# Kernel optimization log

Hardware: AMD Instinct MI355X
Metric: run time of the kernel (lower is better)

## Reference

```python
import jax, jax.numpy as jnp
import numpy as np

B, S, H = 32, 4096, 1024


def setup_inputs() -> dict:
    key = jax.random.key(0)
    ks = jax.random.split(key, 6)
    sc = 1.0 / np.sqrt(H)
    return {
        "hidden_state": jax.random.normal(ks[0], (B, 1, H), dtype=jnp.float32),
        "encoder_outputs": jax.random.normal(ks[1], (B, S, H), dtype=jnp.float32),
        "A_w": jax.random.normal(ks[2], (H, H), dtype=jnp.float32) * sc,
        "A_b": jax.random.normal(ks[3], (H,), dtype=jnp.float32) * 0.01,
        "C_w": jax.random.normal(ks[4], (H, 2 * H), dtype=jnp.float32) * sc,
        "C_b": jax.random.normal(ks[5], (H,), dtype=jnp.float32) * 0.01,
    }


def reference(hidden_state, encoder_outputs, A_w, A_b, C_w, C_b):
    # NOTE: source applies A twice to hidden_state (first reassignment, then
    # again inside the bmm). We reproduce that exactly.
    h1 = hidden_state @ A_w.T + A_b            # [B,1,H] (reassigned hidden_state)
    h2 = h1 @ A_w.T + A_b                      # second A application for scores
    scores = jnp.einsum('bsh,bqh->bsq', encoder_outputs, h2)   # [B,S,1]
    attn = jax.nn.softmax(scores, axis=1)                      # softmax over S
    context = jnp.einsum('bsq,bsh->bqh', attn, encoder_outputs)  # [B,1,H]
    concat = jnp.concatenate([h1[:, 0], context[:, 0]], axis=1)  # [B,2H]
    out = jnp.tanh(concat @ C_w.T + C_b)                         # [B,H]
    return out, attn
```

## Files before the change

### kernel.cpp

```cpp
#include <hip/hip_runtime.h>
#include <math.h>

#define B_ 32
#define S_ 4096
#define H_ 1024

#define RPB   64
#define NBLK  (S_ / RPB)
#define RPW   16

__device__ __forceinline__ float wave_reduce_sum(float v) {
    #pragma unroll
    for (int o = 32; o > 0; o >>= 1) v += __shfl_xor(v, o, 64);
    return v;
}

__device__ __forceinline__ void wave_reduce_sum2(float& a, float& b) {
    #pragma unroll
    for (int o = 32; o > 0; o >>= 1) {
        a += __shfl_xor(a, o, 64);
        b += __shfl_xor(b, o, 64);
    }
}

__global__ __launch_bounds__(256) void gemv_aw(const float* __restrict__ x, int xstride,
                                               const float* __restrict__ W,
                                               const float* __restrict__ bias,
                                               float* __restrict__ y, int ystride) {
    int w = threadIdx.x >> 6, lane = threadIdx.x & 63;
    int gw = blockIdx.x * 4 + w;
    int b = gw >> 7;
    int i0 = (gw & 127) << 3;
    const float4* xr = reinterpret_cast<const float4*>(x + (size_t)b * xstride);
    float4 xv[4];
    #pragma unroll
    for (int k = 0; k < 4; ++k) xv[k] = xr[lane + k * 64];
    #pragma unroll
    for (int j = 0; j < 8; j += 2) {
        const float4* w0 = reinterpret_cast<const float4*>(W + (size_t)(i0 + j) * H_);
        const float4* w1 = reinterpret_cast<const float4*>(W + (size_t)(i0 + j + 1) * H_);
        float s0 = 0.f, s1 = 0.f;
        #pragma unroll
        for (int k = 0; k < 4; ++k) {
            float4 a = w0[lane + k * 64], c = w1[lane + k * 64];
            s0 += a.x * xv[k].x + a.y * xv[k].y + a.z * xv[k].z + a.w * xv[k].w;
            s1 += c.x * xv[k].x + c.y * xv[k].y + c.z * xv[k].z + c.w * xv[k].w;
        }
        wave_reduce_sum2(s0, s1);
        if (lane == 0) {
            y[(size_t)b * ystride + i0 + j]     = s0 + bias[i0 + j];
            y[(size_t)b * ystride + i0 + j + 1] = s1 + bias[i0 + j + 1];
        }
    }
}

#define LOADPAIR(d0, d1, r) do {                                                 \
    const float4* rp_ = base + (size_t)(r) * 256;                                \
    d0[0] = rp_[0]; d0[1] = rp_[64]; d0[2] = rp_[128]; d0[3] = rp_[192];         \
    const float4* rq_ = rp_ + 256;                                               \
    d1[0] = rq_[0]; d1[1] = rq_[64]; d1[2] = rq_[128]; d1[3] = rq_[192];         \
} while (0)

#define PROCESS(va, vb, lr) do {                                                 \
    float s0 = 0.f, s1 = 0.f;                                                    \
    _Pragma("unroll")                                                            \
    for (int k = 0; k < 4; ++k) {                                                \
        s0 += va[k].x * hv[k].x + va[k].y * hv[k].y + va[k].z * hv[k].z + va[k].w * hv[k].w; \
        s1 += vb[k].x * hv[k].x + vb[k].y * hv[k].y + vb[k].z * hv[k].z + vb[k].w * hv[k].w; \
    }                                                                            \
    wave_reduce_sum2(s0, s1);                                                    \
    my_score = (lane == (lr)    ) ? s0 : my_score;                               \
    my_score = (lane == (lr) + 1) ? s1 : my_score;                               \
    float tm_ = fmaxf(s0, s1);                                                   \
    if (tm_ > m) {                                       \
        float sc_ = __expf(m - tm_);          \
        l *= sc_;                                                                \
        _Pragma("unroll")                                                        \
        for (int k = 0; k < 4; ++k) {                                            \
            acc[k].x *= sc_; acc[k].y *= sc_; acc[k].z *= sc_; acc[k].w *= sc_;  \
        }                                                                        \
        m = tm_;                                                                 \
    }                                                                            \
    float p0_ = __expf(s0 - m), p1_ = __expf(s1 - m);                            \
    l += p0_ + p1_;                                                              \
    _Pragma("unroll")                                                            \
    for (int k = 0; k < 4; ++k) {                                                \
        acc[k].x += p0_ * va[k].x + p1_ * vb[k].x;                               \
        acc[k].y += p0_ * va[k].y + p1_ * vb[k].y;                               \
        acc[k].z += p0_ * va[k].z + p1_ * vb[k].z;                               \
        acc[k].w += p0_ * va[k].w + p1_ * vb[k].w;                               \
    }                                                                            \
} while (0)

__global__ __launch_bounds__(256, 3) void attn_pass1(const float* __restrict__ enc,
                                                     const float* __restrict__ h2,
                                                     float* __restrict__ scores,
                                                     float* __restrict__ partials) {
    int b   = blockIdx.x >> 6;
    int blk = blockIdx.x & (NBLK - 1);
    int w = threadIdx.x >> 6, lane = threadIdx.x & 63;

    int row0 = blk * RPB + w * RPW;
    const float4* base = reinterpret_cast<const float4*>(
        enc + (size_t)b * S_ * H_ + (size_t)row0 * H_) + lane;

    const float4* hp = reinterpret_cast<const float4*>(h2 + (size_t)b * H_);
    float4 hv[4];
    #pragma unroll
    for (int k = 0; k < 4; ++k) hv[k] = hp[lane + k * 64];

    float m = -INFINITY, l = 0.f;
    float4 acc[4];
    #pragma unroll
    for (int k = 0; k < 4; ++k) acc[k] = make_float4(0.f, 0.f, 0.f, 0.f);
    float my_score = 0.f;

    float4 A0[4], A1[4], B0[4], B1[4];
    LOADPAIR(A0, A1, 0);
    LOADPAIR(B0, B1, 2);

    #pragma unroll 1
    for (int t = 0; t < RPW; t += 4) {
        PROCESS(A0, A1, t);
        if (t + 4 < RPW) LOADPAIR(A0, A1, t + 4);
        PROCESS(B0, B1, t + 2);
        if (t + 6 < RPW) LOADPAIR(B0, B1, t + 6);
    }
    if (lane < RPW) scores[(size_t)b * S_ + row0 + lane] = my_score;

    __shared__ float lds_ctx[4][H_];
    __shared__ float lds_m[4], lds_l[4];
    float4* mc = reinterpret_cast<float4*>(&lds_ctx[w][0]);
    #pragma unroll
    for (int k = 0; k < 4; ++k) mc[lane + k * 64] = acc[k];
    if (lane == 0) { lds_m[w] = m; lds_l[w] = l; }
    __syncthreads();

    float mb = fmaxf(fmaxf(lds_m[0], lds_m[1]), fmaxf(lds_m[2], lds_m[3]));
    float sc0 = __expf(lds_m[0] - mb), sc1 = __expf(lds_m[1] - mb);
    float sc2 = __expf(lds_m[2] - mb), sc3 = __expf(lds_m[3] - mb);
    float lb = lds_l[0] * sc0 + lds_l[1] * sc1 + lds_l[2] * sc2 + lds_l[3] * sc3;

    float* part = partials + ((size_t)b * NBLK + blk) * (H_ + 2);
    #pragma unroll
    for (int k2 = 0; k2 < 4; ++k2) {
        int col = threadIdx.x + k2 * 256;
        float v = lds_ctx[0][col] * sc0 + lds_ctx[1][col] * sc1 +
                  lds_ctx[2][col] * sc2 + lds_ctx[3][col] * sc3;
        part[2 + col] = v;
    }
    if (threadIdx.x == 0) { part[0] = mb; part[1] = lb; }
}

__global__ __launch_bounds__(256) void attn_reduce(const float* __restrict__ partials,
                                                   float* __restrict__ concat,
                                                   const float* __restrict__ scores,
                                                   float* __restrict__ attn_out) {
    int b = blockIdx.x >> 2;
    int q = blockIdx.x & 3;
    const float* part = partials + (size_t)b * NBLK * (H_ + 2);
    __shared__ float s_m[NBLK], s_l[NBLK], s_sc[NBLK];
    int t = threadIdx.x;
    if (t < NBLK) {
        s_m[t] = part[(size_t)t * (H_ + 2)];
        s_l[t] = part[(size_t)t * (H_ + 2) + 1];
    }
    __syncthreads();
    float mb = -INFINITY;
    #pragma unroll
    for (int k = 0; k < NBLK; ++k) mb = fmaxf(mb, s_m[k]);
    if (t < NBLK) s_sc[t] = __expf(s_m[t] - mb);
    __syncthreads();
    float lb = 0.f;
    #pragma unroll
    for (int k = 0; k < NBLK; ++k) lb += s_l[k] * s_sc[k];
    float inv_l = 1.f / lb;
    int col = q * 256 + t;
    float v = 0.f;
    #pragma unroll 8
    for (int k = 0; k < NBLK; ++k)
        v += part[(size_t)k * (H_ + 2) + 2 + col] * s_sc[k];
    concat[(size_t)b * 2048 + 1024 + col] = v * inv_l;

    const float4* sp = reinterpret_cast<const float4*>(scores + (size_t)b * S_ + q * 1024);
    float4* ap = reinterpret_cast<float4*>(attn_out + (size_t)b * S_ + q * 1024);
    float4 sv = sp[t];
    float4 av;
    av.x = __expf(sv.x - mb) * inv_l;
    av.y = __expf(sv.y - mb) * inv_l;
    av.z = __expf(sv.z - mb) * inv_l;
    av.w = __expf(sv.w - mb) * inv_l;
    ap[t] = av;
}

__global__ __launch_bounds__(256) void out_gemm(const float* __restrict__ concat,
                                                const float* __restrict__ Cw,
                                                const float* __restrict__ Cb,
                                                float* __restrict__ out) {
    int w = threadIdx.x >> 6, lane = threadIdx.x & 63;
    int i = blockIdx.x;
    const float4* wr = reinterpret_cast<const float4*>(Cw + (size_t)i * 2048);
    float4 wv[8];
    #pragma unroll
    for (int k = 0; k < 8; ++k) wv[k] = wr[lane + k * 64];
    float bias = Cb[i];
    #pragma unroll
    for (int bb = 0; bb < 8; ++bb) {
        int b = w * 8 + bb;
        const float4* cr = reinterpret_cast<const float4*>(concat + (size_t)b * 2048);
        float s = 0.f;
        #pragma unroll
        for (int k = 0; k < 8; ++k) {
            float4 c = cr[lane + k * 64];
            s += c.x * wv[k].x + c.y * wv[k].y + c.z * wv[k].z + c.w * wv[k].w;
        }
        s = wave_reduce_sum(s);
        if (lane == 0) out[(size_t)b * H_ + i] = tanhf(s + bias);
    }
}

extern "C" void kernel_launch(void* const* d_in, const int* in_sizes, int n_in,
                              void* d_out, int out_size, void* d_ws, size_t ws_size,
                              hipStream_t stream) {
    const float* hs  = (const float*)d_in[0];
    const float* enc = (const float*)d_in[1];
    const float* A_w = (const float*)d_in[2];
    const float* A_b = (const float*)d_in[3];
    const float* C_w = (const float*)d_in[4];
    const float* C_b = (const float*)d_in[5];

    float* out      = (float*)d_out;
    float* attn_out = out + B_ * H_;

    float* ws       = (float*)d_ws;
    float* concat   = ws;
    float* h2       = ws + (size_t)B_ * 2048;
    float* scores   = h2 + (size_t)B_ * H_;
    float* partials = scores + (size_t)B_ * S_;

    gemv_aw<<<(B_ * H_) / 32, 256, 0, stream>>>(hs, H_, A_w, A_b, concat, 2048);
    gemv_aw<<<(B_ * H_) / 32, 256, 0, stream>>>(concat, 2048, A_w, A_b, h2, H_);
    attn_pass1<<<B_ * NBLK, 256, 0, stream>>>(enc, h2, scores, partials);
    attn_reduce<<<B_ * 4, 256, 0, stream>>>(partials, concat, scores, attn_out);
    out_gemm<<<H_, 256, 0, stream>>>(concat, C_w, C_b, out);
}
```

Before: 143.9 us.

## Stride rows across blocks, use nontemporal loads, four-deep single-row pipeline

```diff
diff --git a/kernel.cpp b/kernel.cpp
--- a/kernel.cpp
+++ b/kernel.cpp
@@ -5,9 +5,14 @@
 #define S_ 4096
 #define H_ 1024
 
-#define RPB   64
-#define NBLK  (S_ / RPB)
+#define NBLK  64
 #define RPW   16
+
+typedef float f32x4 __attribute__((ext_vector_type(4)));
+__device__ __forceinline__ float4 ntload(const float4* p) {
+    f32x4 v = __builtin_nontemporal_load(reinterpret_cast<const f32x4*>(p));
+    union { f32x4 a; float4 b; } u; u.a = v; return u.b;
+}
 
 __device__ __forceinline__ float wave_reduce_sum(float v) {
     #pragma unroll
@@ -54,45 +59,40 @@
     }
 }
 
-#define LOADPAIR(d0, d1, r) do {                                                 \
-    const float4* rp_ = base + (size_t)(r) * 256;                                \
-    d0[0] = rp_[0]; d0[1] = rp_[64]; d0[2] = rp_[128]; d0[3] = rp_[192];         \
-    const float4* rq_ = rp_ + 256;                                               \
-    d1[0] = rq_[0]; d1[1] = rq_[64]; d1[2] = rq_[128]; d1[3] = rq_[192];         \
+#define LOADROW1(dst, t) do {                                                    \
+    const float4* rp_ = base + (size_t)(t) * 65536;                              \
+    dst[0] = ntload(rp_);       dst[1] = ntload(rp_ + 64);                       \
+    dst[2] = ntload(rp_ + 128); dst[3] = ntload(rp_ + 192);                      \
 } while (0)
 
-#define PROCESS(va, vb, lr) do {                                                 \
-    float s0 = 0.f, s1 = 0.f;                                                    \
+#define PROCESS1(va, t) do {                                                     \
+    float s_ = 0.f;                                                              \
     _Pragma("unroll")                                                            \
-    for (int k = 0; k < 4; ++k) {                                                \
-        s0 += va[k].x * hv[k].x + va[k].y * hv[k].y + va[k].z * hv[k].z + va[k].w * hv[k].w; \
-        s1 += vb[k].x * hv[k].x + vb[k].y * hv[k].y + vb[k].z * hv[k].z + vb[k].w * hv[k].w; \
-    }                                                                            \
-    wave_reduce_sum2(s0, s1);                                                    \
-    my_score = (lane == (lr)    ) ? s0 : my_score;                               \
-    my_score = (lane == (lr) + 1) ? s1 : my_score;                               \
-    float tm_ = fmaxf(s0, s1);                                                   \
-    if (tm_ > m) {                                       \
-        float sc_ = __expf(m - tm_);          \
+    for (int k = 0; k < 4; ++k)                                                  \
+        s_ += va[k].x * hv[k].x + va[k].y * hv[k].y + va[k].z * hv[k].z + va[k].w * hv[k].w; \
+    s_ = wave_reduce_sum(s_);                                                    \
+    my_score = (lane == (t)) ? s_ : my_score;                                    \
+    if (s_ > m) {                                              \
+        float sc_ = __expf(m - s_);           \
         l *= sc_;                                                                \
         _Pragma("unroll")                                                        \
         for (int k = 0; k < 4; ++k) {                                            \
             acc[k].x *= sc_; acc[k].y *= sc_; acc[k].z *= sc_; acc[k].w *= sc_;  \
         }                                                                        \
-        m = tm_;                                                                 \
+        m = s_;                                                                  \
     }                                                                            \
-    float p0_ = __expf(s0 - m), p1_ = __expf(s1 - m);                            \
-    l += p0_ + p1_;                                                              \
+    float p_ = __expf(s_ - m);                                                   \
+    l += p_;                                                                     \
     _Pragma("unroll")                                                            \
     for (int k = 0; k < 4; ++k) {                                                \
-        acc[k].x += p0_ * va[k].x + p1_ * vb[k].x;                               \
-        acc[k].y += p0_ * va[k].y + p1_ * vb[k].y;                               \
-        acc[k].z += p0_ * va[k].z + p1_ * vb[k].z;                               \
-        acc[k].w += p0_ * va[k].w + p1_ * vb[k].w;                               \
+        acc[k].x += p_ * va[k].x;                                                \
+        acc[k].y += p_ * va[k].y;                                                \
+        acc[k].z += p_ * va[k].z;                                                \
+        acc[k].w += p_ * va[k].w;                                                \
     }                                                                            \
 } while (0)
 
-__global__ __launch_bounds__(256, 3) void attn_pass1(const float* __restrict__ enc,
+__global__ __launch_bounds__(256, 4) void attn_pass1(const float* __restrict__ enc,
                                                      const float* __restrict__ h2,
                                                      float* __restrict__ scores,
                                                      float* __restrict__ partials) {
@@ -100,9 +100,8 @@
     int blk = blockIdx.x & (NBLK - 1);
     int w = threadIdx.x >> 6, lane = threadIdx.x & 63;
 
-    int row0 = blk * RPB + w * RPW;
     const float4* base = reinterpret_cast<const float4*>(
-        enc + (size_t)b * S_ * H_ + (size_t)row0 * H_) + lane;
+        enc + (size_t)b * S_ * H_ + (size_t)(blk + 64 * w) * H_) + lane;
 
     const float4* hp = reinterpret_cast<const float4*>(h2 + (size_t)b * H_);
     float4 hv[4];
@@ -115,18 +114,17 @@
     for (int k = 0; k < 4; ++k) acc[k] = make_float4(0.f, 0.f, 0.f, 0.f);
     float my_score = 0.f;
 
-    float4 A0[4], A1[4], B0[4], B1[4];
-    LOADPAIR(A0, A1, 0);
-    LOADPAIR(B0, B1, 2);
+    float4 A[4], B[4], C[4], D[4];
+    LOADROW1(A, 0); LOADROW1(B, 1); LOADROW1(C, 2); LOADROW1(D, 3);
 
     #pragma unroll 1
     for (int t = 0; t < RPW; t += 4) {
-        PROCESS(A0, A1, t);
-        if (t + 4 < RPW) LOADPAIR(A0, A1, t + 4);
-        PROCESS(B0, B1, t + 2);
-        if (t + 6 < RPW) LOADPAIR(B0, B1, t + 6);
-    }
-    if (lane < RPW) scores[(size_t)b * S_ + row0 + lane] = my_score;
+        PROCESS1(A, t);     if (t + 4 < RPW) LOADROW1(A, t + 4);
+        PROCESS1(B, t + 1); if (t + 5 < RPW) LOADROW1(B, t + 5);
+        PROCESS1(C, t + 2); if (t + 6 < RPW) LOADROW1(C, t + 6);
+        PROCESS1(D, t + 3); if (t + 7 < RPW) LOADROW1(D, t + 7);
+    }
+    if (lane < RPW) scores[(size_t)b * S_ + blk + 64 * (w + 4 * lane)] = my_score;
 
     __shared__ float lds_ctx[4][H_];
     __shared__ float lds_m[4], lds_l[4];
```

Measured after the change: 179.1 us. +24.5%, slower.
